# Optimization experiments

Measured on AMD Instinct MI355X. Metric: run time of the kernel, lower is better.

The kernel has to match this reference:

```python
import jax, jax.numpy as jnp
import numpy as np

N = 100000
E = 1600000
IN_C, HID_C, OUT_C = 128, 256, 64
EPS = 1e-5


def _glorot(key, shape):
    fan_in, fan_out = shape
    lim = float(np.sqrt(6.0 / (fan_in + fan_out)))
    return jax.random.uniform(key, shape, jnp.float32, -lim, lim)


def sage_conv(x, src, dst, deg_inv, W_l, b_l, W_r):
    # mean aggregation of neighbor features into target nodes
    msg_sum = jax.ops.segment_sum(x[src], dst, num_segments=N)  # [N, d]
    mean = msg_sum * deg_inv[:, None]
    return mean @ W_l + b_l + x @ W_r


def batch_norm(x, gamma, beta, rm, rv):
    return (x - rm) * jax.lax.rsqrt(rv + EPS) * gamma + beta


def setup_inputs() -> dict:
    key = jax.random.key(0)
    ks = jax.random.split(key, 10)
    x = jax.random.normal(ks[0], (N, IN_C), jnp.float32)
    edge_index = jax.random.randint(ks[1], (2, E), 0, N, jnp.int64)
    inp = {
        "x": x,
        "edge_index": edge_index,
        # layer 1: SAGEConv(IN_C -> HID_C) + BN
        "W1l": _glorot(ks[2], (IN_C, HID_C)),
        "b1l": jnp.zeros((HID_C,), jnp.float32),
        "W1r": _glorot(ks[3], (IN_C, HID_C)),
        "g1": jnp.ones((HID_C,), jnp.float32),
        "be1": jnp.zeros((HID_C,), jnp.float32),
        "rm1": 0.1 * jax.random.normal(ks[4], (HID_C,), jnp.float32),
        "rv1": jnp.ones((HID_C,), jnp.float32),
        # layer 2: SAGEConv(HID_C -> HID_C) + BN
        "W2l": _glorot(ks[5], (HID_C, HID_C)),
        "b2l": jnp.zeros((HID_C,), jnp.float32),
        "W2r": _glorot(ks[6], (HID_C, HID_C)),
        "g2": jnp.ones((HID_C,), jnp.float32),
        "be2": jnp.zeros((HID_C,), jnp.float32),
        "rm2": 0.1 * jax.random.normal(ks[7], (HID_C,), jnp.float32),
        "rv2": jnp.ones((HID_C,), jnp.float32),
        # classifier: SAGEConv(HID_C -> OUT_C)
        "Wcl": _glorot(ks[8], (HID_C, OUT_C)),
        "bcl": jnp.zeros((OUT_C,), jnp.float32),
        "Wcr": _glorot(ks[9], (HID_C, OUT_C)),
    }
    return inp


def reference(x, edge_index, W1l, b1l, W1r, g1, be1, rm1, rv1,
              W2l, b2l, W2r, g2, be2, rm2, rv2, Wcl, bcl, Wcr):
    src, dst = edge_index[0], edge_index[1]
    deg = jax.ops.segment_sum(jnp.ones((E,), jnp.float32), dst, num_segments=N)
    deg_inv = jnp.where(deg > 0, 1.0 / jnp.maximum(deg, 1.0), 0.0)

    h = sage_conv(x, src, dst, deg_inv, W1l, b1l, W1r)
    h = jax.nn.relu(batch_norm(h, g1, be1, rm1, rv1))
    # dropout is identity in eval mode (training=False)
    h = sage_conv(h, src, dst, deg_inv, W2l, b2l, W2r)
    h = jax.nn.relu(batch_norm(h, g2, be2, rm2, rv2))
    return sage_conv(h, src, dst, deg_inv, Wcl, bcl, Wcr)
```

## Files before the change

kernel.cpp:

```cpp
#include <hip/hip_runtime.h>
#include <stdint.h>

#define NN 100000
#define EE 1600000
#define IN_C 128
#define HID_C 256
#define OUT_C 64

#define NB 391
#define CAP 5120
#define K3_NPT 25
#define K3_BLOCKS 250

typedef unsigned short bf16_t;
typedef unsigned int u32;
typedef __attribute__((ext_vector_type(8))) short bf16x8;
typedef __attribute__((ext_vector_type(4))) float f32x4;

__device__ __forceinline__ float b2f(unsigned short u){
  unsigned int x = ((unsigned int)u) << 16;
  return __uint_as_float(x);
}
__device__ __forceinline__ unsigned short f2b(float f){
  unsigned int x = __float_as_uint(f);
  unsigned int r = x + 0x7FFFu + ((x >> 16) & 1u);
  return (unsigned short)(r >> 16);
}

__global__ void detect_edge_k(const int* __restrict__ ei, int* __restrict__ eflag){
  __shared__ int sm[256];
  int t = threadIdx.x;
  int o = 0;
  for (int i = t; i < 1024; i += 256) o |= ei[2*i + 1];
  sm[t] = o; __syncthreads();
  for (int s = 128; s > 0; s >>= 1){
    if (t < s) sm[t] |= sm[t + s];
    __syncthreads();
  }
  if (t == 0) *eflag = (sm[0] == 0) ? 1 : 0;
}

__global__ __launch_bounds__(256) void bcount_k(const int* __restrict__ ei,
    const int* __restrict__ eflag, int* __restrict__ bcnt){
  __shared__ int h[NB];
  int t = threadIdx.x;
  for (int i = t; i < NB; i += 256) h[i] = 0;
  __syncthreads();
  int i64 = *eflag;
  int base = blockIdx.x * (256 * K3_NPT);
  #pragma unroll
  for (int q = 0; q < K3_NPT; ++q){
    int e = base + q * 256 + t;
    int d = i64 ? ei[2*(EE + e)] : ei[EE + e];
    atomicAdd(&h[d >> 8], 1);
  }
  __syncthreads();
  for (int i = t; i < NB; i += 256) if (h[i]) atomicAdd(&bcnt[i], h[i]);
}

__global__ void bscan_k(const int* __restrict__ bcnt, int* __restrict__ bbase){
  __shared__ int sm[512];
  int t = threadIdx.x;
  sm[t] = (t < NB) ? bcnt[t] : 0;
  __syncthreads();
  for (int off = 1; off < 512; off <<= 1){
    int a = (t >= off) ? sm[t - off] : 0;
    __syncthreads();
    sm[t] += a;
    __syncthreads();
  }
  if (t <= NB) bbase[t] = (t == 0) ? 0 : sm[t - 1];
}

__global__ __launch_bounds__(256) void bscatter_k(const int* __restrict__ ei,
    const int* __restrict__ eflag, const int* __restrict__ bbase,
    int* __restrict__ bfill, uint2* __restrict__ pairs){
  __shared__ int cnt[NB];
  __shared__ int cnt2[NB];
  __shared__ int lbase[NB];
  int t = threadIdx.x;
  for (int i = t; i < NB; i += 256){ cnt[i] = 0; cnt2[i] = 0; }
  __syncthreads();
  int i64 = *eflag;
  int ebase = blockIdx.x * (256 * K3_NPT);
  int src[K3_NPT], dst[K3_NPT];
  #pragma unroll
  for (int q = 0; q < K3_NPT; ++q){
    int e = ebase + q * 256 + t;
    src[q] = i64 ? ei[2*e] : ei[e];
    dst[q] = i64 ? ei[2*(EE + e)] : ei[EE + e];
    atomicAdd(&cnt[dst[q] >> 8], 1);
  }
  __syncthreads();
  for (int i = t; i < NB; i += 256)
    lbase[i] = cnt[i] ? atomicAdd(&bfill[i], cnt[i]) : 0;
  __syncthreads();
  #pragma unroll
  for (int q = 0; q < K3_NPT; ++q){
    int b = dst[q] >> 8;
    int r = atomicAdd(&cnt2[b], 1);
    pairs[bbase[b] + lbase[b] + r] = make_uint2((u32)src[q], (u32)dst[q]);
  }
}

__global__ __launch_bounds__(256) void bsort_k(const uint2* __restrict__ pairs,
    const int* __restrict__ bbase, int* __restrict__ rowptr, int* __restrict__ csr){
  __shared__ int hist[256];
  __shared__ int pref[257];
  __shared__ int cnt[256];
  __shared__ int lsrc[CAP];
  int b = blockIdx.x;
  int t = threadIdx.x;
  int e0 = bbase[b], e1 = bbase[b + 1];
  int s = e1 - e0;
  hist[t] = 0; cnt[t] = 0;
  __syncthreads();
  for (int i = t; i < s; i += 256)
    atomicAdd(&hist[pairs[e0 + i].y & 255], 1);
  __syncthreads();
  for (int off = 1; off < 256; off <<= 1){
    int a = (t >= off) ? hist[t - off] : 0;
    __syncthreads();
    hist[t] += a;
    __syncthreads();
  }
  if (t == 0) pref[0] = 0;
  pref[t + 1] = hist[t];
  __syncthreads();
  int gid = b * 256 + t;
  if (gid <= NN) rowptr[gid] = e0 + pref[t];
  for (int i = t; i < s; i += 256){
    uint2 p = pairs[e0 + i];
    int bin = p.y & 255;
    int r = atomicAdd(&cnt[bin], 1);
    int pos = pref[bin] + r;
    if (pos < CAP) lsrc[pos] = (int)p.x;
    else           csr[e0 + pos] = (int)p.x;
  }
  __syncthreads();
  int lim = s < CAP ? s : CAP;
  for (int i = t; i < lim; i += 256) csr[e0 + i] = lsrc[i];
}


__global__ void f2b_vec_k(const float* __restrict__ in, bf16_t* __restrict__ out, int n){
  int g = blockIdx.x * 256 + threadIdx.x;
  int i = g * 4;
  if (i < n){
    float4 v = *(const float4*)(in + i);
    uint2 u;
    u.x = (u32)f2b(v.x) | ((u32)f2b(v.y) << 16);
    u.y = (u32)f2b(v.z) | ((u32)f2b(v.w) << 16);
    *(uint2*)(out + i) = u;
  }
}

struct WtArgs {
  const float* W[6];
  bf16_t* Wt[6];
  int K[6], N[6];
  int off[7];
};

__global__ void wt_all_k(WtArgs a){
  int g = blockIdx.x * 256 + threadIdx.x;
  if (g >= a.off[6]) return;
  #pragma unroll
  for (int s = 0; s < 6; ++s){
    if (g >= a.off[s] && g < a.off[s + 1]){
      int local = g - a.off[s];
      int K = a.K[s], N = a.N[s];
      int n = local / K, k = local - n * K;
      a.Wt[s][local] = f2b(a.W[s][(size_t)k * N + n]);
    }
  }
}


template<int C, bool SIGNED, typename TIN>
__global__ __launch_bounds__(256) void quant_k(const TIN* __restrict__ in,
    uint8_t* __restrict__ outq, float* __restrict__ scales){
  constexpr int V = C / 64;
  int row  = (blockIdx.x * 256 + threadIdx.x) >> 6;
  int lane = threadIdx.x & 63;
  if (row >= NN) return;
  float v[V];
  if constexpr (sizeof(TIN) == 4){
    float2 u = *(const float2*)((const float*)in + (size_t)row * C + lane * 2);
    v[0] = u.x; v[1] = u.y;
  } else {
    const bf16_t* bp = (const bf16_t*)in + (size_t)row * C + lane * V;
    if constexpr (V == 4){
      uint2 u = *(const uint2*)bp;
      v[0] = b2f((unsigned short)(u.x & 0xffffu)); v[1] = b2f((unsigned short)(u.x >> 16));
      v[2] = b2f((unsigned short)(u.y & 0xffffu)); v[3] = b2f((unsigned short)(u.y >> 16));
    } else if constexpr (V == 2){
      u32 u = *(const u32*)bp;
      v[0] = b2f((unsigned short)(u & 0xffffu)); v[1] = b2f((unsigned short)(u >> 16));
    } else {
      v[0] = b2f(*bp);
    }
  }
  float m = 0.f;
  #pragma unroll
  for (int i = 0; i < V; ++i) m = fmaxf(m, SIGNED ? fabsf(v[i]) : v[i]);
  #pragma unroll
  for (int msk = 1; msk < 64; msk <<= 1) m = fmaxf(m, __shfl_xor(m, msk, 64));
  const float qmax = SIGNED ? 127.f : 255.f;
  float inv = m > 0.f ? qmax / m : 0.f;
  uint8_t qb[V];
  #pragma unroll
  for (int i = 0; i < V; ++i){
    float qf = rintf(v[i] * inv);
    if (SIGNED){
      qf = fminf(fmaxf(qf, -127.f), 127.f);
      qb[i] = (uint8_t)(int8_t)(int)qf;
    } else {
      qf = fminf(fmaxf(qf, 0.f), 255.f);
      qb[i] = (uint8_t)(int)qf;
    }
  }
  uint8_t* op = outq + (size_t)row * C + lane * V;
  if constexpr (V == 4){
    u32 p = (u32)qb[0] | ((u32)qb[1] << 8) | ((u32)qb[2] << 16) | ((u32)qb[3] << 24);
    *(u32*)op = p;
  } else if constexpr (V == 2){
    *(unsigned short*)op = (unsigned short)((u32)qb[0] | ((u32)qb[1] << 8));
  } else {
    *op = qb[0];
  }
  if (lane == 0) scales[row] = m / qmax;
}


__device__ __forceinline__ float qdec(u32 w, int b, bool sgn){
  u32 byte = (w >> (8 * b)) & 0xffu;
  return sgn ? (float)(int8_t)byte : (float)byte;
}

template<int C, bool SIGNED>
__global__ __launch_bounds__(256) void agg_q8_k(const uint8_t* __restrict__ tq,
    const float* __restrict__ tsc,
    const int* __restrict__ rowptr, const int* __restrict__ csr,
    bf16_t* __restrict__ outm){
  constexpr int V = C / 64;
  int wid  = (blockIdx.x * 256 + threadIdx.x) >> 6;
  int lane = threadIdx.x & 63;
  if (wid >= NN) return;
  int beg = __builtin_amdgcn_readfirstlane(rowptr[wid]);
  int end = __builtin_amdgcn_readfirstlane(rowptr[wid + 1]);
  float acc[V];
  #pragma unroll
  for (int i = 0; i < V; ++i) acc[i] = 0.f;

  const uint8_t* hb = tq + lane * V;
  int e = beg;
  for (; e + 7 < end; e += 8){
    int   s[8]; float sc[8];
    #pragma unroll
    for (int q = 0; q < 8; ++q) s[q] = csr[e + q];
    u32 w[8];
    #pragma unroll
    for (int q = 0; q < 8; ++q){
      if constexpr (V == 4) w[q] = *(const u32*)(hb + (size_t)s[q] * C);
      else                  w[q] = *(const unsigned short*)(hb + (size_t)s[q] * C);
      sc[q] = tsc[s[q]];
    }
    #pragma unroll
    for (int q = 0; q < 8; ++q)
      #pragma unroll
      for (int i = 0; i < V; ++i)
        acc[i] += sc[q] * qdec(w[q], i, SIGNED);
  }
  for (; e < end; ++e){
    int s0 = csr[e];
    u32 w0;
    if constexpr (V == 4) w0 = *(const u32*)(hb + (size_t)s0 * C);
    else                  w0 = *(const unsigned short*)(hb + (size_t)s0 * C);
    float sc0 = tsc[s0];
    #pragma unroll
    for (int i = 0; i < V; ++i) acc[i] += sc0 * qdec(w0, i, SIGNED);
  }

  int d = end - beg;
  float di = d > 0 ? 1.0f / (float)d : 0.f;
  bf16_t* po = outm + (size_t)wid * C + lane * V;
  if constexpr (V == 2){
    u32 u = (u32)f2b(acc[0] * di) | ((u32)f2b(acc[1] * di) << 16);
    *(u32*)po = u;
  } else {
    uint2 u;
    u.x = (u32)f2b(acc[0] * di) | ((u32)f2b(acc[1] * di) << 16);
    u.y = (u32)f2b(acc[2] * di) | ((u32)f2b(acc[3] * di) << 16);
    *(uint2*)po = u;
  }
}


__global__ __launch_bounds__(256) void agg_final_q8_k(
    const uint8_t* __restrict__ Pq, const float* __restrict__ scp,
    const float* __restrict__ Q,
    const int* __restrict__ rowptr, const int* __restrict__ csr,
    float* __restrict__ out){
  int wid  = (blockIdx.x * 256 + threadIdx.x) >> 6;
  int lane = threadIdx.x & 63;
  if (wid >= NN) return;
  int beg = __builtin_amdgcn_readfirstlane(rowptr[wid]);
  int end = __builtin_amdgcn_readfirstlane(rowptr[wid + 1]);
  const uint8_t* Pb = Pq + lane;
  float acc = 0.f;
  int e = beg;
  for (; e + 7 < end; e += 8){
    int s[8]; uint8_t b[8]; float sc[8];
    #pragma unroll
    for (int q = 0; q < 8; ++q) s[q] = csr[e + q];
    #pragma unroll
    for (int q = 0; q < 8; ++q){ b[q] = Pb[(size_t)s[q] * 64]; sc[q] = scp[s[q]]; }
    #pragma unroll
    for (int q = 0; q < 8; ++q) acc += sc[q] * (float)(int8_t)b[q];
  }
  for (; e < end; ++e) acc += scp[csr[e]] * (float)(int8_t)Pb[(size_t)csr[e] * 64];
  int d = end - beg;
  float di = d > 0 ? 1.0f / (float)d : 0.f;
  out[(size_t)wid * 64 + lane] = acc * di + Q[(size_t)wid * 64 + lane];
}


template<int BN, int NT_N>
__global__ __launch_bounds__(256) void mfma_gemm_k(
    const bf16_t* __restrict__ A0, const bf16_t* __restrict__ A1,
    const bf16_t* __restrict__ W0t, const bf16_t* __restrict__ W1t,
    const float* __restrict__ bias,
    const float* __restrict__ gamma, const float* __restrict__ beta,
    const float* __restrict__ rmean, const float* __restrict__ rvar,
    bf16_t* __restrict__ out, int M, int K, int Nout)
{
  constexpr int BM = 128;
  constexpr int BK = 64;
  constexpr int LDA = BK + 8;
  __shared__ bf16_t As[BM * LDA];
  __shared__ bf16_t Bs[BN * LDA];

  int t    = threadIdx.x;
  int lane = t & 63;
  int wid  = t >> 6;
  int wr   = wid >> 1, wc = wid & 1;
  int l15  = lane & 15;
  int quad = lane >> 4;

  int m0 = blockIdx.x * BM;
  int n0 = blockIdx.y * BN;

  f32x4 acc[4][NT_N];
  #pragma unroll
  for (int i = 0; i < 4; ++i)
    #pragma unroll
    for (int j = 0; j < NT_N; ++j)
      acc[i][j] = (f32x4){0.f, 0.f, 0.f, 0.f};

  for (int pass = 0; pass < 2; ++pass){
    const bf16_t* A  = pass ? A1 : A0;
    const bf16_t* Wt = pass ? W1t : W0t;
    for (int k0 = 0; k0 < K; k0 += BK){
      #pragma unroll
      for (int i = 0; i < (BM * (BK/8)) / 256; ++i){
        int c = t + i * 256;
        int row = c >> 3, k8 = c & 7;
        uint4 v = make_uint4(0u, 0u, 0u, 0u);
        int gm = m0 + row;
        if (gm < M) v = *(const uint4*)(A + (size_t)gm * K + k0 + k8 * 8);
        *(uint4*)(As + row * LDA + k8 * 8) = v;
      }
      #pragma unroll
      for (int i = 0; i < (BN * (BK/8)) / 256; ++i){
        int c = t + i * 256;
        int row = c >> 3, k8 = c & 7;
        uint4 v = *(const uint4*)(Wt + (size_t)(n0 + row) * K + k0 + k8 * 8);
        *(uint4*)(Bs + row * LDA + k8 * 8) = v;
      }
      __syncthreads();
      #pragma unroll
      for (int kk = 0; kk < BK; kk += 32){
        bf16x8 af[4], bfr[NT_N];
        #pragma unroll
        for (int i = 0; i < 4; ++i)
          af[i] = *(const bf16x8*)(As + (wr * 64 + i * 16 + l15) * LDA + kk + quad * 8);
        #pragma unroll
        for (int j = 0; j < NT_N; ++j)
          bfr[j] = *(const bf16x8*)(Bs + (wc * (NT_N * 16) + j * 16 + l15) * LDA + kk + quad * 8);
        #pragma unroll
        for (int i = 0; i < 4; ++i)
          #pragma unroll
          for (int j = 0; j < NT_N; ++j)
            acc[i][j] = __builtin_amdgcn_mfma_f32_16x16x32_bf16(af[i], bfr[j], acc[i][j], 0, 0, 0);
      }
      __syncthreads();
    }
  }

  #pragma unroll
  for (int j = 0; j < NT_N; ++j){
    int col = n0 + wc * (NT_N * 16) + j * 16 + l15;
    float sc = gamma[col] * rsqrtf(rvar[col] + 1e-5f);
    float shift = (bias[col] - rmean[col]) * sc + beta[col];
    #pragma unroll
    for (int i = 0; i < 4; ++i){
      int rbase = m0 + wr * 64 + i * 16 + quad * 4;
      #pragma unroll
      for (int r = 0; r < 4; ++r){
        int row = rbase + r;
        if (row < M){
          float v = fmaxf(acc[i][j][r] * sc + shift, 0.f);
          out[(size_t)row * Nout + col] = f2b(v);
        }
      }
    }
  }
}


__global__ __launch_bounds__(256) void gemm3_k(
    const bf16_t* __restrict__ A, const bf16_t* __restrict__ Wt,
    const float* __restrict__ bcl,
    bf16_t* __restrict__ P, float* __restrict__ Q, int M)
{
  constexpr int BM = 128, BN = 128, BK = 64, K = 256;
  constexpr int LDA = BK + 8;
  __shared__ bf16_t As[BM * LDA];
  __shared__ bf16_t Bs[BN * LDA];

  int t    = threadIdx.x;
  int lane = t & 63;
  int wid  = t >> 6;
  int wr   = wid >> 1, wc = wid & 1;
  int l15  = lane & 15;
  int quad = lane >> 4;
  int m0 = blockIdx.x * BM;

  f32x4 acc[4][4];
  #pragma unroll
  for (int i = 0; i < 4; ++i)
    #pragma unroll
    for (int j = 0; j < 4; ++j)
      acc[i][j] = (f32x4){0.f, 0.f, 0.f, 0.f};

  for (int k0 = 0; k0 < K; k0 += BK){
    #pragma unroll
    for (int i = 0; i < 4; ++i){
      int c = t + i * 256;
      int row = c >> 3, k8 = c & 7;
      uint4 v = make_uint4(0u, 0u, 0u, 0u);
      int gm = m0 + row;
      if (gm < M) v = *(const uint4*)(A + (size_t)gm * K + k0 + k8 * 8);
      *(uint4*)(As + row * LDA + k8 * 8) = v;
    }
    #pragma unroll
    for (int i = 0; i < 4; ++i){
      int c = t + i * 256;
      int row = c >> 3, k8 = c & 7;
      uint4 v = *(const uint4*)(Wt + (size_t)row * K + k0 + k8 * 8);
      *(uint4*)(Bs + row * LDA + k8 * 8) = v;
    }
    __syncthreads();
    #pragma unroll
    for (int kk = 0; kk < BK; kk += 32){
      bf16x8 af[4], bfr[4];
      #pragma unroll
      for (int i = 0; i < 4; ++i)
        af[i] = *(const bf16x8*)(As + (wr * 64 + i * 16 + l15) * LDA + kk + quad * 8);
      #pragma unroll
      for (int j = 0; j < 4; ++j)
        bfr[j] = *(const bf16x8*)(Bs + (wc * 64 + j * 16 + l15) * LDA + kk + quad * 8);
      #pragma unroll
      for (int i = 0; i < 4; ++i)
        #pragma unroll
        for (int j = 0; j < 4; ++j)
          acc[i][j] = __builtin_amdgcn_mfma_f32_16x16x32_bf16(af[i], bfr[j], acc[i][j], 0, 0, 0);
    }
    __syncthreads();
  }

  #pragma unroll
  for (int j = 0; j < 4; ++j){
    int col = wc * 64 + j * 16 + l15;
    #pragma unroll
    for (int i = 0; i < 4; ++i){
      int rbase = m0 + wr * 64 + i * 16 + quad * 4;
      #pragma unroll
      for (int r = 0; r < 4; ++r){
        int row = rbase + r;
        if (row < M){
          float v = acc[i][j][r];
          if (col < 64) P[(size_t)row * 64 + col] = f2b(v);
          else          Q[(size_t)row * 64 + (col - 64)] = v + bcl[col - 64];
        }
      }
    }
  }
}


extern "C" void kernel_launch(void* const* d_in, const int* in_sizes, int n_in,
                              void* d_out, int out_size, void* d_ws, size_t ws_size,
                              hipStream_t stream)
{
  const float* x   = (const float*)d_in[0];
  const int*   ei  = (const int*)d_in[1];
  const float* W1l = (const float*)d_in[2];
  const float* b1l = (const float*)d_in[3];
  const float* W1r = (const float*)d_in[4];
  const float* g1  = (const float*)d_in[5];
  const float* be1 = (const float*)d_in[6];
  const float* rm1 = (const float*)d_in[7];
  const float* rv1 = (const float*)d_in[8];
  const float* W2l = (const float*)d_in[9];
  const float* b2l = (const float*)d_in[10];
  const float* W2r = (const float*)d_in[11];
  const float* g2  = (const float*)d_in[12];
  const float* be2 = (const float*)d_in[13];
  const float* rm2 = (const float*)d_in[14];
  const float* rv2 = (const float*)d_in[15];
  const float* Wcl = (const float*)d_in[16];
  const float* bcl = (const float*)d_in[17];
  const float* Wcr = (const float*)d_in[18];
  (void)in_sizes; (void)n_in; (void)out_size; (void)ws_size;

  char* ws = (char*)d_ws;
  size_t off = 0;
  auto alloc = [&](size_t bytes)->char* {
    char* p = ws + off;
    off += (bytes + 15) & ~(size_t)15;
    return p;
  };
  int*    bcnt   = (int*)   alloc(800 * 4);
  int*    bfill  = bcnt + 400;
  int*    bbase  = (int*)   alloc((size_t)(NB + 1) * 4);
  int*    rowptr = (int*)   alloc((size_t)(NN + 1) * 4);
  int*    eflag  = (int*)   alloc(16);
  int*    csr    = (int*)   alloc((size_t)EE * 4);
  bf16_t* xb     = (bf16_t*)alloc((size_t)NN * IN_C * 2);
  bf16_t* aggb   = (bf16_t*)alloc((size_t)NN * HID_C * 2);
  bf16_t* h1     = (bf16_t*)alloc((size_t)NN * HID_C * 2);
  bf16_t* h2     = (bf16_t*)alloc((size_t)NN * HID_C * 2);
  bf16_t* W1lt   = (bf16_t*)alloc((size_t)IN_C  * HID_C * 2);
  bf16_t* W1rt   = (bf16_t*)alloc((size_t)IN_C  * HID_C * 2);
  bf16_t* W2lt   = (bf16_t*)alloc((size_t)HID_C * HID_C * 2);
  bf16_t* W2rt   = (bf16_t*)alloc((size_t)HID_C * HID_C * 2);
  bf16_t* Wc3t   = (bf16_t*)alloc((size_t)128 * HID_C * 2);
  float*  sc1    = (float*) alloc((size_t)NN * 4);
  float*  scp    = (float*) alloc((size_t)NN * 4);

  uint2*   pairs = (uint2*)aggb;
  uint8_t* xq  = (uint8_t*)h2;
  float*   scx = (float*)((char*)h2 + (size_t)NN * IN_C);
  uint8_t* h1q = (uint8_t*)xb;
  bf16_t*  P   = xb;
  uint8_t* Pq  = (uint8_t*)aggb;
  float*   Q   = (float*)h1;

  hipMemsetAsync(bcnt, 0, 800 * 4, stream);

  f2b_vec_k<<<(NN * IN_C / 4 + 255) / 256, 256, 0, stream>>>(x, xb, NN * IN_C);
  WtArgs wa;
  wa.W[0] = W1l; wa.Wt[0] = W1lt; wa.K[0] = IN_C;  wa.N[0] = HID_C;
  wa.W[1] = W1r; wa.Wt[1] = W1rt; wa.K[1] = IN_C;  wa.N[1] = HID_C;
  wa.W[2] = W2l; wa.Wt[2] = W2lt; wa.K[2] = HID_C; wa.N[2] = HID_C;
  wa.W[3] = W2r; wa.Wt[3] = W2rt; wa.K[3] = HID_C; wa.N[3] = HID_C;
  wa.W[4] = Wcl; wa.Wt[4] = Wc3t;             wa.K[4] = HID_C; wa.N[4] = OUT_C;
  wa.W[5] = Wcr; wa.Wt[5] = Wc3t + 64 * 256;  wa.K[5] = HID_C; wa.N[5] = OUT_C;
  wa.off[0] = 0;
  for (int s = 0; s < 6; ++s) wa.off[s + 1] = wa.off[s] + wa.K[s] * wa.N[s];
  wt_all_k<<<(wa.off[6] + 255) / 256, 256, 0, stream>>>(wa);

  detect_edge_k<<<1, 256, 0, stream>>>(ei, eflag);
  bcount_k<<<K3_BLOCKS, 256, 0, stream>>>(ei, eflag, bcnt);
  bscan_k<<<1, 512, 0, stream>>>(bcnt, bbase);
  bscatter_k<<<K3_BLOCKS, 256, 0, stream>>>(ei, eflag, bbase, bfill, pairs);
  bsort_k<<<NB, 256, 0, stream>>>(pairs, bbase, rowptr, csr);

  int wb = (NN + 3) / 4;
  int mblocks = (NN + 127) / 128;

  quant_k<IN_C, true, float><<<wb, 256, 0, stream>>>(x, xq, scx);
  agg_q8_k<IN_C, true><<<wb, 256, 0, stream>>>(xq, scx, rowptr, csr, aggb);
  dim3 g1d(mblocks, HID_C / 128);
  mfma_gemm_k<128, 4><<<g1d, 256, 0, stream>>>(
      aggb, xb, W1lt, W1rt, b1l, g1, be1, rm1, rv1, h1, NN, IN_C, HID_C);

  quant_k<HID_C, false, bf16_t><<<wb, 256, 0, stream>>>(h1, h1q, sc1);
  agg_q8_k<HID_C, false><<<wb, 256, 0, stream>>>(h1q, sc1, rowptr, csr, aggb);
  mfma_gemm_k<128, 4><<<g1d, 256, 0, stream>>>(
      aggb, h1, W2lt, W2rt, b2l, g2, be2, rm2, rv2, h2, NN, HID_C, HID_C);

  gemm3_k<<<mblocks, 256, 0, stream>>>(h2, Wc3t, bcl, P, Q, NN);
  quant_k<OUT_C, true, bf16_t><<<wb, 256, 0, stream>>>(P, Pq, scp);
  agg_final_q8_k<<<wb, 256, 0, stream>>>(Pq, scp, Q, rowptr, csr, (float*)d_out);
}
```

Measured before the change: 612.5 us.

## Double-buffer GEMM tiles with direct global-to-LDS loads and XOR swizzle

The three MFMA GEMM kernels now stage A and B tiles straight from global memory into LDS with global_load_lds, which skips the register round trip. Two LDS buffers let the next tile load while the current one is multiplied, synchronised by manual vmcnt waits and raw barriers. A padded layout is replaced by an XOR swizzle to avoid bank conflicts. Out-of-range rows are clamped rather than zeroed, and the pipeline depends on hand-counted vmcnt values staying correct.

```diff
diff --git a/kernel.cpp b/kernel.cpp
--- a/kernel.cpp
+++ b/kernel.cpp
@@ -26,6 +26,10 @@
   unsigned int r = x + 0x7FFFu + ((x >> 16) & 1u);
   return (unsigned short)(r >> 16);
 }
+
+#define GL16(gp, lp) __builtin_amdgcn_global_load_lds( \
+    (const __attribute__((address_space(1))) void*)(gp), \
+    (__attribute__((address_space(3))) void*)(lp), 16, 0, 0)
 
 __global__ void detect_edge_k(const int* __restrict__ ei, int* __restrict__ eflag){
   __shared__ int sm[256];
@@ -326,20 +330,22 @@
 }
 
 
-template<int BN, int NT_N>
+template<int K_>
 __global__ __launch_bounds__(256) void mfma_gemm_k(
     const bf16_t* __restrict__ A0, const bf16_t* __restrict__ A1,
     const bf16_t* __restrict__ W0t, const bf16_t* __restrict__ W1t,
     const float* __restrict__ bias,
     const float* __restrict__ gamma, const float* __restrict__ beta,
     const float* __restrict__ rmean, const float* __restrict__ rvar,
-    bf16_t* __restrict__ out, int M, int K, int Nout)
+    bf16_t* __restrict__ out, int M, int Nout)
 {
   constexpr int BM = 128;
+  constexpr int BN = 128;
   constexpr int BK = 64;
-  constexpr int LDA = BK + 8;
-  __shared__ bf16_t As[BM * LDA];
-  __shared__ bf16_t Bs[BN * LDA];
+  constexpr int KT = K_ / BK;
+  constexpr int T  = 2 * KT;
+  __shared__ bf16_t As[2][BM * BK];
+  __shared__ bf16_t Bs[2][BN * BK];
 
   int t    = threadIdx.x;
   int lane = t & 63;
@@ -351,56 +357,70 @@
   int m0 = blockIdx.x * BM;
   int n0 = blockIdx.y * BN;
 
-  f32x4 acc[4][NT_N];
+  f32x4 acc[4][4];
   #pragma unroll
   for (int i = 0; i < 4; ++i)
     #pragma unroll
-    for (int j = 0; j < NT_N; ++j)
+    for (int j = 0; j < 4; ++j)
       acc[i][j] = (f32x4){0.f, 0.f, 0.f, 0.f};
 
-  for (int pass = 0; pass < 2; ++pass){
-    const bf16_t* A  = pass ? A1 : A0;
-    const bf16_t* Wt = pass ? W1t : W0t;
-    for (int k0 = 0; k0 < K; k0 += BK){
-      #pragma unroll
-      for (int i = 0; i < (BM * (BK/8)) / 256; ++i){
-        int c = t + i * 256;
-        int row = c >> 3, k8 = c & 7;
-        uint4 v = make_uint4(0u, 0u, 0u, 0u);
-        int gm = m0 + row;
-        if (gm < M) v = *(const uint4*)(A + (size_t)gm * K + k0 + k8 * 8);
-        *(uint4*)(As + row * LDA + k8 * 8) = v;
+  auto stage = [&](int tile, int buf){
+    const bf16_t* Ap = (tile < KT) ? A0 : A1;
+    const bf16_t* Wp = (tile < KT) ? W0t : W1t;
+    int k0 = ((tile < KT) ? tile : tile - KT) * BK;
+    #pragma unroll
+    for (int i = 0; i < 4; ++i){
+      int c   = i * 256 + t;
+      int row = c >> 3;
+      int k8  = (c & 7) ^ (row & 7);
+      int gm  = m0 + row; gm = gm < NN ? gm : NN - 1;
+      GL16(Ap + (size_t)gm * K_ + k0 + k8 * 8, &As[buf][(i * 256 + (t & 192)) * 8]);
+    }
+    #pragma unroll
+    for (int i = 0; i < 4; ++i){
+      int c   = i * 256 + t;
+      int row = c >> 3;
+      int k8  = (c & 7) ^ (row & 7);
+      GL16(Wp + (size_t)(n0 + row) * K_ + k0 + k8 * 8, &Bs[buf][(i * 256 + (t & 192)) * 8]);
+    }
+  };
+
+  stage(0, 0);
+  #pragma unroll
+  for (int tile = 0; tile < T; ++tile){
+    int buf = tile & 1;
+    if (tile + 1 < T){
+      stage(tile + 1, buf ^ 1);
+      asm volatile("s_waitcnt vmcnt(8)" ::: "memory");
+    } else {
+      asm volatile("s_waitcnt vmcnt(0)" ::: "memory");
+    }
+    __builtin_amdgcn_s_barrier();
+    #pragma unroll
+    for (int kk = 0; kk < 2; ++kk){
+      bf16x8 af[4], bfr[4];
+      #pragma unroll
+      for (int i = 0; i < 4; ++i){
+        int row = wr * 64 + i * 16 + l15;
+        af[i] = *(const bf16x8*)(&As[buf][(size_t)((row << 3) + ((quad + kk * 4) ^ (row & 7))) * 8]);
       }
       #pragma unroll
-      for (int i = 0; i < (BN * (BK/8)) / 256; ++i){
-        int c = t + i * 256;
-        int row = c >> 3, k8 = c & 7;
-        uint4 v = *(const uint4*)(Wt + (size_t)(n0 + row) * K + k0 + k8 * 8);
-        *(uint4*)(Bs + row * LDA + k8 * 8) = v;
+      for (int j = 0; j < 4; ++j){
+        int row = wc * 64 + j * 16 + l15;
+        bfr[j] = *(const bf16x8*)(&Bs[buf][(size_t)((row << 3) + ((quad + kk * 4) ^ (row & 7))) * 8]);
       }
-      __syncthreads();
-      #pragma unroll
-      for (int kk = 0; kk < BK; kk += 32){
-        bf16x8 af[4], bfr[NT_N];
+      #pragma unroll
+      for (int i = 0; i < 4; ++i)
         #pragma unroll
-        for (int i = 0; i < 4; ++i)
-          af[i] = *(const bf16x8*)(As + (wr * 64 + i * 16 + l15) * LDA + kk + quad * 8);
-        #pragma unroll
-        for (int j = 0; j < NT_N; ++j)
-          bfr[j] = *(const bf16x8*)(Bs + (wc * (NT_N * 16) + j * 16 + l15) * LDA + kk + quad * 8);
-        #pragma unroll
-        for (int i = 0; i < 4; ++i)
-          #pragma unroll
-          for (int j = 0; j < NT_N; ++j)
-            acc[i][j] = __builtin_amdgcn_mfma_f32_16x16x32_bf16(af[i], bfr[j], acc[i][j], 0, 0, 0);
-      }
-      __syncthreads();
-    }
-  }
-
-  #pragma unroll
-  for (int j = 0; j < NT_N; ++j){
-    int col = n0 + wc * (NT_N * 16) + j * 16 + l15;
+        for (int j = 0; j < 4; ++j)
+          acc[i][j] = __builtin_amdgcn_mfma_f32_16x16x32_bf16(af[i], bfr[j], acc[i][j], 0, 0, 0);
+    }
+    __builtin_amdgcn_s_barrier();
+  }
+
+  #pragma unroll
+  for (int j = 0; j < 4; ++j){
+    int col = n0 + wc * 64 + j * 16 + l15;
     float sc = gamma[col] * rsqrtf(rvar[col] + 1e-5f);
     float shift = (bias[col] - rmean[col]) * sc + beta[col];
     #pragma unroll
@@ -424,10 +444,10 @@
     const float* __restrict__ bcl,
     bf16_t* __restrict__ P, float* __restrict__ Q, int M)
 {
-  constexpr int BM = 128, BN = 128, BK = 64, K = 256;
-  constexpr int LDA = BK + 8;
-  __shared__ bf16_t As[BM * LDA];
-  __shared__ bf16_t Bs[BN * LDA];
+  constexpr int K_ = 256, BM = 128, BN = 128, BK = 64;
+  constexpr int T = K_ / BK;
+  __shared__ bf16_t As[2][BM * BK];
+  __shared__ bf16_t Bs[2][BN * BK];
 
   int t    = threadIdx.x;
   int lane = t & 63;
@@ -444,40 +464,56 @@
     for (int j = 0; j < 4; ++j)
       acc[i][j] = (f32x4){0.f, 0.f, 0.f, 0.f};
 
-  for (int k0 = 0; k0 < K; k0 += BK){
+  auto stage = [&](int tile, int buf){
+    int k0 = tile * BK;
     #pragma unroll
     for (int i = 0; i < 4; ++i){
-      int c = t + i * 256;
-      int row = c >> 3, k8 = c & 7;
-      uint4 v = make_uint4(0u, 0u, 0u, 0u);
-      int gm = m0 + row;
-      if (gm < M) v = *(const uint4*)(A + (size_t)gm * K + k0 + k8 * 8);
-      *(uint4*)(As + row * LDA + k8 * 8) = v;
+      int c   = i * 256 + t;
+      int row = c >> 3;
+      int k8  = (c & 7) ^ (row & 7);
+      int gm  = m0 + row; gm = gm < NN ? gm : NN - 1;
+      GL16(A + (size_t)gm * K_ + k0 + k8 * 8, &As[buf][(i * 256 + (t & 192)) * 8]);
     }
     #pragma unroll
     for (int i = 0; i < 4; ++i){
-      int c = t + i * 256;
-      int row = c >> 3, k8 = c & 7;
-      uint4 v = *(const uint4*)(Wt + (size_t)row * K + k0 + k8 * 8);
-      *(uint4*)(Bs + row * LDA + k8 * 8) = v;
-    }
-    __syncthreads();
-    #pragma unroll
-    for (int kk = 0; kk < BK; kk += 32){
+      int c   = i * 256 + t;
+      int row = c >> 3;
+      int k8  = (c & 7) ^ (row & 7);
+      GL16(Wt + (size_t)row * K_ + k0 + k8 * 8, &Bs[buf][(i * 256 + (t & 192)) * 8]);
+    }
+  };
+
+  stage(0, 0);
+  #pragma unroll
+  for (int tile = 0; tile < T; ++tile){
+    int buf = tile & 1;
+    if (tile + 1 < T){
+      stage(tile + 1, buf ^ 1);
+      asm volatile("s_waitcnt vmcnt(8)" ::: "memory");
+    } else {
+      asm volatile("s_waitcnt vmcnt(0)" ::: "memory");
+    }
+    __builtin_amdgcn_s_barrier();
+    #pragma unroll
+    for (int kk = 0; kk < 2; ++kk){
       bf16x8 af[4], bfr[4];
       #pragma unroll
-      for (int i = 0; i < 4; ++i)
-        af[i] = *(const bf16x8*)(As + (wr * 64 + i * 16 + l15) * LDA + kk + quad * 8);
-      #pragma unroll
-      for (int j = 0; j < 4; ++j)
-        bfr[j] = *(const bf16x8*)(Bs + (wc * 64 + j * 16 + l15) * LDA + kk + quad * 8);
+      for (int i = 0; i < 4; ++i){
+        int row = wr * 64 + i * 16 + l15;
+        af[i] = *(const bf16x8*)(&As[buf][(size_t)((row << 3) + ((quad + kk * 4) ^ (row & 7))) * 8]);
+      }
+      #pragma unroll
+      for (int j = 0; j < 4; ++j){
+        int row = wc * 64 + j * 16 + l15;
+        bfr[j] = *(const bf16x8*)(&Bs[buf][(size_t)((row << 3) + ((quad + kk * 4) ^ (row & 7))) * 8]);
+      }
       #pragma unroll
       for (int i = 0; i < 4; ++i)
         #pragma unroll
         for (int j = 0; j < 4; ++j)
           acc[i][j] = __builtin_amdgcn_mfma_f32_16x16x32_bf16(af[i], bfr[j], acc[i][j], 0, 0, 0);
     }
-    __syncthreads();
+    __builtin_amdgcn_s_barrier();
   }
 
   #pragma unroll
@@ -584,13 +620,13 @@
   quant_k<IN_C, true, float><<<wb, 256, 0, stream>>>(x, xq, scx);
   agg_q8_k<IN_C, true><<<wb, 256, 0, stream>>>(xq, scx, rowptr, csr, aggb);
   dim3 g1d(mblocks, HID_C / 128);
-  mfma_gemm_k<128, 4><<<g1d, 256, 0, stream>>>(
-      aggb, xb, W1lt, W1rt, b1l, g1, be1, rm1, rv1, h1, NN, IN_C, HID_C);
+  mfma_gemm_k<IN_C><<<g1d, 256, 0, stream>>>(
+      aggb, xb, W1lt, W1rt, b1l, g1, be1, rm1, rv1, h1, NN, HID_C);
 
   quant_k<HID_C, false, bf16_t><<<wb, 256, 0, stream>>>(h1, h1q, sc1);
   agg_q8_k<HID_C, false><<<wb, 256, 0, stream>>>(h1q, sc1, rowptr, csr, aggb);
-  mfma_gemm_k<128, 4><<<g1d, 256, 0, stream>>>(
-      aggb, h1, W2lt, W2rt, b2l, g2, be2, rm2, rv2, h2, NN, HID_C, HID_C);
+  mfma_gemm_k<HID_C><<<g1d, 256, 0, stream>>>(
+      aggb, h1, W2lt, W2rt, b2l, g2, be2, rm2, rv2, h2, NN, HID_C);
 
   gemm3_k<<<mblocks, 256, 0, stream>>>(h2, Wc3t, bcl, P, Q, NN);
   quant_k<OUT_C, true, bf16_t><<<wb, 256, 0, stream>>>(P, Pq, scp);
```

Result: faster. 589.5 us (-3.8%).
